# Performance work log

Hardware: AMD Instinct MI355X
Metric: run time of the kernel (lower is better)

Reference implementation:

```python
import jax, jax.numpy as jnp
import numpy as np

NUM_HEADS = 32
HEAD_DIM = 128
NUM_KV_HEADS = 8
SCALE = HEAD_DIM ** -0.5
SNAPKV_LIMIT = 512   # context.snapkv_limit
SAMPLE_Q = 128       # context.snapkv_sample_queries default
B = 4                # number of sequences (uniform length)
L = 1024             # tokens per sequence
NUM_SLOTS = 8192
NEG = jnp.float32(-1e30)


def setup_inputs() -> dict:
    key = jax.random.key(0)
    k0, k1, k2 = jax.random.split(key, 3)
    N = B * L
    q = jax.random.normal(k0, (N, NUM_HEADS, HEAD_DIM), jnp.float32)
    k = jax.random.normal(k1, (N, NUM_KV_HEADS, HEAD_DIM), jnp.float32)
    v = jax.random.normal(k2, (N, NUM_KV_HEADS, HEAD_DIM), jnp.float32)
    D = NUM_KV_HEADS * HEAD_DIM
    k_cache = jnp.zeros((NUM_SLOTS, D), jnp.float32)
    v_cache = jnp.zeros((NUM_SLOTS, D), jnp.float32)
    slot_mapping = jnp.arange(N, dtype=jnp.int32)
    cu_seqlens = jnp.arange(B + 1, dtype=jnp.int32) * L
    return dict(q=q, k=k, v=v, k_cache=k_cache, v_cache=v_cache,
                slot_mapping=slot_mapping, cu_seqlens=cu_seqlens)


def _forward(q, k, v, k_cache, v_cache, slot_mapping, cu_seqlens):
    N, H, Dh = q.shape
    Hkv = k.shape[1]
    rep = H // Hkv
    nb = cu_seqlens.shape[0] - 1
    Ls = N // nb  # uniform seq length
    qb = q.reshape(nb, Ls, H, Dh)
    kb = k.reshape(nb, Ls, Hkv, Dh)
    vb = v.reshape(nb, Ls, Hkv, Dh)

    # ---- SnapKV selection (per sequence, vectorized over batch) ----
    q_s = qb[:, Ls - SAMPLE_Q:]                       # [B, SQ, H, Dh] last queries
    k_rep = jnp.repeat(kb, rep, axis=2)               # GQA expand -> [B, L, H, Dh]
    logits = jnp.einsum('bqhd,bkhd->bhqk', q_s, k_rep) * SCALE
    abs_q = jnp.arange(Ls - SAMPLE_Q, Ls)
    abs_k = jnp.arange(Ls)
    allowed = abs_k[None, :] <= abs_q[:, None]        # [SQ, L] causal for sampled q
    logits = jnp.where(allowed[None, None], logits, NEG)
    attn = jax.nn.softmax(logits, axis=-1)
    importance = attn.sum(axis=(1, 2))                # [B, L] sum over heads+queries
    _, idx = jax.lax.top_k(importance, SNAPKV_LIMIT)
    keep_idx = jnp.sort(idx, axis=-1)                 # [B, limit] sorted kept positions

    # ---- compact KV-cache store (store_kvcache on kept tokens) ----
    kept_k = jnp.take_along_axis(kb, keep_idx[:, :, None, None], axis=1)  # [B,limit,Hkv,Dh]
    kept_v = jnp.take_along_axis(vb, keep_idx[:, :, None, None], axis=1)
    # compact slots: first num_kept (= limit) slots of each sequence
    slots = slot_mapping.reshape(nb, Ls)[:, :SNAPKV_LIMIT].reshape(-1)
    D = Hkv * Dh
    k_cache_new = k_cache.at[slots].set(kept_k.reshape(-1, D))
    v_cache_new = v_cache.at[slots].set(kept_v.reshape(-1, D))

    # ---- prefill attention (flash_attn_varlen_func, causal, raw k/v) ----
    v_rep = jnp.repeat(vb, rep, axis=2)               # [B, L, H, Dh]
    scores = jnp.einsum('bqhd,bkhd->bhqk', qb, k_rep) * SCALE
    causal = abs_k[None, :] <= abs_k[:, None]         # [L, L]
    scores = jnp.where(causal[None, None], scores, NEG)
    p = jax.nn.softmax(scores, axis=-1)
    o = jnp.einsum('bhqk,bkhd->bqhd', p, v_rep).reshape(N, H, Dh)
    return o, k_cache_new, v_cache_new


def reference(q, k, v, k_cache, v_cache, slot_mapping, cu_seqlens):
    return _forward(q, k, v, k_cache, v_cache, slot_mapping, cu_seqlens)
```

## Files before the change

kernel.cpp:

```cpp
#include <hip/hip_runtime.h>

#define B_ 4
#define L_ 1024
#define H_ 32
#define HKV_ 8
#define DH_ 128
#define SCALE_ 0.08838834764831845f
#define M_FIX 20.0f
#define KEEP_ 512
#define O_ELEMS (B_*L_*H_*DH_)
#define CACHE_ELEMS (8192*HKV_*DH_)
#define TILE_US 8192
#define QTAB_US 2097152

typedef short short8 __attribute__((ext_vector_type(8)));
typedef float floatx4 __attribute__((ext_vector_type(4)));
typedef unsigned int uintx2 __attribute__((ext_vector_type(2)));
typedef unsigned int uintx4 __attribute__((ext_vector_type(4)));

__device__ inline unsigned short bf16r(float x) {
    unsigned int u = __builtin_bit_cast(unsigned int, x);
    u += 0x7fffu + ((u >> 16) & 1u);
    return (unsigned short)(u >> 16);
}
__device__ inline unsigned int pk_bf16(float a, float b) {
    return (unsigned int)bf16r(a) | ((unsigned int)bf16r(b) << 16);
}
__device__ inline float bf16tof(unsigned short h) {
    unsigned int u = ((unsigned int)h) << 16;
    return __builtin_bit_cast(float, u);
}

__global__ __launch_bounds__(256)
void convert_kernel(const float* __restrict__ Kp, const float* __restrict__ Vp,
                    const float* __restrict__ Qp,
                    unsigned short* __restrict__ Kb, unsigned short* __restrict__ Klo,
                    unsigned short* __restrict__ VTb,
                    unsigned short* __restrict__ Qh, unsigned short* __restrict__ Ql)
{
    int bid = blockIdx.x;
    int kt = bid & 15, hkv = (bid >> 4) & 7, b = bid >> 7;
    int t = threadIdx.x;
    size_t tile = (size_t)bid * TILE_US;

    #pragma unroll
    for (int i = 0; i < 4; ++i) {
        int pos = t + 256 * i;
        int col = pos >> 4, gd = pos & 15;
        const float* kb = &Kp[((size_t)(b * L_ + kt * 64 + col) * HKV_ + hkv) * DH_ + gd * 8];
        float x[8];
        *(float4*)&x[0] = *(const float4*)kb;
        *(float4*)&x[4] = *(const float4*)(kb + 4);
        unsigned int gh[4], gl[4];
        #pragma unroll
        for (int j = 0; j < 4; ++j) {
            unsigned short h0 = bf16r(x[2*j]),   h1 = bf16r(x[2*j+1]);
            unsigned short l0 = bf16r(x[2*j]   - bf16tof(h0));
            unsigned short l1 = bf16r(x[2*j+1] - bf16tof(h1));
            gh[j] = (unsigned int)h0 | ((unsigned int)h1 << 16);
            gl[j] = (unsigned int)l0 | ((unsigned int)l1 << 16);
        }
        int phys = gd ^ (col & 15);
        *(uintx4*)&Kb[tile + col * 128 + phys * 8]  = (uintx4){gh[0], gh[1], gh[2], gh[3]};
        *(uintx4*)&Klo[tile + col * 128 + phys * 8] = (uintx4){gl[0], gl[1], gl[2], gl[3]};
    }

    {
        int d4g = t & 31, g = t >> 5;
        const float* vb = &Vp[((size_t)(b * L_ + kt * 64 + g * 8) * HKV_ + hkv) * DH_ + d4g * 4];
        const size_t vs = (size_t)HKV_ * DH_;
        float4 r[8];
        #pragma unroll
        for (int j = 0; j < 8; ++j) r[j] = *(const float4*)(vb + (size_t)j * vs);
        #pragma unroll
        for (int ii = 0; ii < 4; ++ii) {
            int d = d4g * 4 + ii;
            int phys = g ^ (d & 7);
            uintx4 gp;
            gp[0] = pk_bf16(((const float*)&r[0])[ii], ((const float*)&r[1])[ii]);
            gp[1] = pk_bf16(((const float*)&r[2])[ii], ((const float*)&r[3])[ii]);
            gp[2] = pk_bf16(((const float*)&r[4])[ii], ((const float*)&r[5])[ii]);
            gp[3] = pk_bf16(((const float*)&r[6])[ii], ((const float*)&r[7])[ii]);
            *(uintx4*)&VTb[tile + d * 64 + phys * 8] = gp;
        }
    }

    if (bid < 256) {
        int qts = bid & 1;
        int h   = (bid >> 1) & 31;
        int qb_ = bid >> 6;
        int w = t >> 6, l = t & 63, lm = l & 15, hq = l >> 4;
        int q0 = 896 + qts * 64;
        const float* qb = Qp + ((size_t)(qb_ * L_ + q0 + w * 16 + lm) * H_ + h) * DH_;
        #pragma unroll
        for (int c = 0; c < 4; ++c) {
            int dc = hq * 8 + 32 * c;
            float x[8];
            *(float4*)&x[0] = *(const float4*)(qb + dc);
            *(float4*)&x[4] = *(const float4*)(qb + dc + 4);
            short8 fh, fl;
            #pragma unroll
            for (int j = 0; j < 8; ++j) {
                float xs = x[j] * SCALE_;
                unsigned short hb = bf16r(xs);
                fh[j] = (short)hb;
                fl[j] = (short)bf16r(xs - bf16tof(hb));
            }
            size_t idx = (((size_t)bid * 4 + c) * 256 + t) * 8;
            *(short8*)&Qh[idx] = fh;
            *(short8*)&Ql[idx] = fl;
        }
    }
}

__global__ __launch_bounds__(256, 4)
void attn_mfma(const float* __restrict__ Qp, const unsigned short* __restrict__ Kbp,
               const unsigned short* __restrict__ VTp, float* __restrict__ Op)
{
    __shared__ __align__(16) unsigned short k_lds[64 * 128];
    __shared__ __align__(16) unsigned short vT[128 * 64];
    __shared__ __align__(16) unsigned short p_lds[4 * 1024];

    int bid = blockIdx.x;
    int pr = bid & 7;
    int h  = (bid >> 3) & 31;
    int b  = bid >> 8;
    int hkv = h >> 2;
    int t = threadIdx.x;
    int w = t >> 6;
    int l = t & 63;
    int lm = l & 15;
    int hq = l >> 4;

    for (int ph = 0; ph < 2; ++ph) {
        int qt = ph ? (15 - pr) : pr;

        short8 aq[4];
        {
            const float* qb = Qp + ((size_t)(b * L_ + qt * 64 + w * 16 + lm) * H_ + h) * DH_;
            #pragma unroll
            for (int c = 0; c < 4; ++c) {
                int dc = hq * 8 + 32 * c;
                float4 x0 = *(const float4*)(qb + dc);
                float4 x1 = *(const float4*)(qb + dc + 4);
                uintx4 packed;
                packed[0] = pk_bf16(x0.x * SCALE_, x0.y * SCALE_);
                packed[1] = pk_bf16(x0.z * SCALE_, x0.w * SCALE_);
                packed[2] = pk_bf16(x1.x * SCALE_, x1.y * SCALE_);
                packed[3] = pk_bf16(x1.z * SCALE_, x1.w * SCALE_);
                aq[c] = __builtin_bit_cast(short8, packed);
            }
        }

        floatx4 O[8];
        #pragma unroll
        for (int n = 0; n < 8; ++n) O[n] = (floatx4){0.f, 0.f, 0.f, 0.f};
        float l_acc[4] = {0.f, 0.f, 0.f, 0.f};

        for (int kt = 0; kt <= qt; ++kt) {
            __syncthreads();
            size_t tbase = (size_t)((b * HKV_ + hkv) * 16 + kt) * TILE_US;
            {
                const uintx4* kg = (const uintx4*)(Kbp + tbase) + t;
                const uintx4* vg = (const uintx4*)(VTp + tbase) + t;
                uintx4* kd = (uintx4*)k_lds + t;
                uintx4* vd = (uintx4*)vT + t;
                #pragma unroll
                for (int i = 0; i < 4; ++i) {
                    kd[i * 256] = kg[i * 256];
                    vd[i * 256] = vg[i * 256];
                }
            }
            __syncthreads();

            floatx4 S[4];
            #pragma unroll
            for (int c = 0; c < 4; ++c) S[c] = (floatx4){-M_FIX, -M_FIX, -M_FIX, -M_FIX};
            #pragma unroll
            for (int kc = 0; kc < 4; ++kc) {
                #pragma unroll
                for (int c = 0; c < 4; ++c) {
                    int row = lm * 4 + c;
                    int phys = (kc * 4 + hq) ^ (row & 15);
                    short8 bk = *(const short8*)&k_lds[row * 128 + phys * 8];
                    S[c] = __builtin_amdgcn_mfma_f32_16x16x32_bf16(aq[kc], bk, S[c], 0, 0, 0);
                }
            }
            bool diag = (kt == qt);
            #pragma unroll
            for (int r = 0; r < 4; ++r) {
                float e0 = __expf(S[0][r]);
                float e1 = __expf(S[1][r]);
                float e2 = __expf(S[2][r]);
                float e3 = __expf(S[3][r]);
                if (diag) {
                    int qabs = qt * 64 + w * 16 + hq * 4 + r;
                    int kb0 = kt * 64 + lm * 4;
                    e0 = (kb0 + 0 <= qabs) ? e0 : 0.f;
                    e1 = (kb0 + 1 <= qabs) ? e1 : 0.f;
                    e2 = (kb0 + 2 <= qabs) ? e2 : 0.f;
                    e3 = (kb0 + 3 <= qabs) ? e3 : 0.f;
                }
                l_acc[r] += (e0 + e1) + (e2 + e3);
                int m = hq * 4 + r;
                int phys = (lm >> 1) ^ (m & 7);
                uintx2 gp;
                gp[0] = pk_bf16(e0, e1);
                gp[1] = pk_bf16(e2, e3);
                *(uintx2*)&p_lds[w * 1024 + m * 64 + phys * 8 + (lm & 1) * 4] = gp;
            }
            asm volatile("" ::: "memory");
            int phys0 = hq ^ (lm & 7);
            int phys1 = (4 + hq) ^ (lm & 7);
            short8 bp0 = *(const short8*)&p_lds[w * 1024 + lm * 64 + phys0 * 8];
            short8 bp1 = *(const short8*)&p_lds[w * 1024 + lm * 64 + phys1 * 8];
            #pragma unroll
            for (int n = 0; n < 8; ++n) {
                int d = n * 16 + lm;
                short8 a0 = *(const short8*)&vT[d * 64 + (hq ^ (d & 7)) * 8];
                O[n] = __builtin_amdgcn_mfma_f32_16x16x32_bf16(a0, bp0, O[n], 0, 0, 0);
                short8 a1 = *(const short8*)&vT[d * 64 + (((4 + hq) ^ (d & 7))) * 8];
                O[n] = __builtin_amdgcn_mfma_f32_16x16x32_bf16(a1, bp1, O[n], 0, 0, 0);
            }
        }
        #pragma unroll
        for (int r = 0; r < 4; ++r) {
            l_acc[r] += __shfl_xor(l_acc[r], 1);
            l_acc[r] += __shfl_xor(l_acc[r], 2);
            l_acc[r] += __shfl_xor(l_acc[r], 4);
            l_acc[r] += __shfl_xor(l_acc[r], 8);
        }
        float* lf = (float*)&p_lds[w * 1024];
        if (lm == 0) {
            #pragma unroll
            for (int r = 0; r < 4; ++r) lf[hq * 4 + r] = l_acc[r];
        }
        asm volatile("" ::: "memory");
        __builtin_amdgcn_wave_barrier();
        float invl = 1.0f / lf[lm];
        #pragma unroll
        for (int n = 0; n < 8; ++n) {
            float4 res;
            res.x = O[n][0] * invl; res.y = O[n][1] * invl;
            res.z = O[n][2] * invl; res.w = O[n][3] * invl;
            *(float4*)&Op[((size_t)(b * L_ + qt * 64 + w * 16 + lm) * H_ + h) * DH_ + n * 16 + hq * 4] = res;
        }
    }
}

__global__ __launch_bounds__(256, 2)
void imp_l_kernel(const unsigned short* __restrict__ Qhp, const unsigned short* __restrict__ Qlp,
                  const unsigned short* __restrict__ Kbp, const unsigned short* __restrict__ Klop,
                  float* __restrict__ invL)
{
    __shared__ __align__(16) unsigned short khi[64 * 128];
    __shared__ __align__(16) unsigned short klo[64 * 128];

    int bid = blockIdx.x;
    int qts = bid & 1;
    int h   = (bid >> 1) & 31;
    int b   = bid >> 6;
    int hkv = h >> 2;
    int t = threadIdx.x;
    int w = t >> 6;
    int l = t & 63;
    int lm = l & 15;
    int hq = l >> 4;
    int q0 = 896 + qts * 64;
    int ktd = q0 >> 6;

    short8 aqh[4], aql[4];
    #pragma unroll
    for (int c = 0; c < 4; ++c) {
        size_t idx = (((size_t)bid * 4 + c) * 256 + t) * 8;
        aqh[c] = *(const short8*)&Qhp[idx];
        aql[c] = *(const short8*)&Qlp[idx];
    }

    float l_acc[4] = {0.f, 0.f, 0.f, 0.f};
    for (int kt = 0; kt <= ktd; ++kt) {
        __syncthreads();
        size_t tbase = (size_t)((b * HKV_ + hkv) * 16 + kt) * TILE_US;
        {
            const uintx4* hg = (const uintx4*)(Kbp + tbase) + t;
            const uintx4* lg = (const uintx4*)(Klop + tbase) + t;
            uintx4* hd = (uintx4*)khi + t;
            uintx4* ld = (uintx4*)klo + t;
            #pragma unroll
            for (int i = 0; i < 4; ++i) {
                hd[i * 256] = hg[i * 256];
                ld[i * 256] = lg[i * 256];
            }
        }
        __syncthreads();

        floatx4 S[4];
        #pragma unroll
        for (int c = 0; c < 4; ++c) S[c] = (floatx4){-M_FIX, -M_FIX, -M_FIX, -M_FIX};
        #pragma unroll
        for (int kc = 0; kc < 4; ++kc) {
            #pragma unroll
            for (int c = 0; c < 4; ++c) {
                int row = lm * 4 + c;
                int phys = (kc * 4 + hq) ^ (row & 15);
                short8 bh = *(const short8*)&khi[row * 128 + phys * 8];
                short8 bl = *(const short8*)&klo[row * 128 + phys * 8];
                S[c] = __builtin_amdgcn_mfma_f32_16x16x32_bf16(aqh[kc], bh, S[c], 0, 0, 0);
                S[c] = __builtin_amdgcn_mfma_f32_16x16x32_bf16(aqh[kc], bl, S[c], 0, 0, 0);
                S[c] = __builtin_amdgcn_mfma_f32_16x16x32_bf16(aql[kc], bh, S[c], 0, 0, 0);
            }
        }
        bool diag = (kt == ktd);
        #pragma unroll
        for (int r = 0; r < 4; ++r) {
            int qabs = q0 + w * 16 + hq * 4 + r;
            #pragma unroll
            for (int c = 0; c < 4; ++c) {
                float ev = __expf(S[c][r]);
                if (diag) {
                    int kabs = kt * 64 + lm * 4 + c;
                    ev = (kabs <= qabs) ? ev : 0.f;
                }
                l_acc[r] += ev;
            }
        }
    }
    #pragma unroll
    for (int r = 0; r < 4; ++r) {
        l_acc[r] += __shfl_xor(l_acc[r], 1);
        l_acc[r] += __shfl_xor(l_acc[r], 2);
        l_acc[r] += __shfl_xor(l_acc[r], 4);
        l_acc[r] += __shfl_xor(l_acc[r], 8);
    }
    if (lm == 0) {
        #pragma unroll
        for (int r = 0; r < 4; ++r)
            invL[((size_t)(b * H_ + h)) * 128 + qts * 64 + w * 16 + hq * 4 + r] = 1.0f / l_acc[r];
    }
}

__global__ __launch_bounds__(256, 4)
void imp_col_kernel(const unsigned short* __restrict__ Qhp, const unsigned short* __restrict__ Qlp,
                    const unsigned short* __restrict__ Kbp, const unsigned short* __restrict__ Klop,
                    const float* __restrict__ invL, float* __restrict__ imp)
{
    __shared__ __align__(16) unsigned short khi[64 * 128];
    __shared__ __align__(16) unsigned short klo[64 * 128];
    __shared__ float imp_loc[64];

    int bid = blockIdx.x;
    int kt = bid & 15;
    int h  = (bid >> 4) & 31;
    int b  = bid >> 9;
    int hkv = h >> 2;
    int t = threadIdx.x;
    int w = t >> 6;
    int l = t & 63;
    int lm = l & 15;
    int hq = l >> 4;

    if (t < 64) imp_loc[t] = 0.f;
    size_t tbase = (size_t)((b * HKV_ + hkv) * 16 + kt) * TILE_US;
    {
        const uintx4* hg = (const uintx4*)(Kbp + tbase) + t;
        const uintx4* lg = (const uintx4*)(Klop + tbase) + t;
        uintx4* hd = (uintx4*)khi + t;
        uintx4* ld = (uintx4*)klo + t;
        #pragma unroll
        for (int i = 0; i < 4; ++i) {
            hd[i * 256] = hg[i * 256];
            ld[i * 256] = lg[i * 256];
        }
    }
    __syncthreads();

    float cs[4] = {0.f, 0.f, 0.f, 0.f};
    for (int qp2 = 0; qp2 < 2; ++qp2) {
        if (kt == 15 && qp2 == 0) continue;
        int q0 = 896 + qp2 * 64;
        int qbid = (b * 32 + h) * 2 + qp2;
        short8 aqh[4], aql[4];
        #pragma unroll
        for (int c = 0; c < 4; ++c) {
            size_t idx = (((size_t)qbid * 4 + c) * 256 + t) * 8;
            aqh[c] = *(const short8*)&Qhp[idx];
            aql[c] = *(const short8*)&Qlp[idx];
        }
        floatx4 iv4 = *(const floatx4*)&invL[((size_t)(b * H_ + h)) * 128 + qp2 * 64 + w * 16 + hq * 4];

        floatx4 S[4];
        #pragma unroll
        for (int c = 0; c < 4; ++c) S[c] = (floatx4){-M_FIX, -M_FIX, -M_FIX, -M_FIX};
        #pragma unroll
        for (int kc = 0; kc < 4; ++kc) {
            #pragma unroll
            for (int c = 0; c < 4; ++c) {
                int row = lm * 4 + c;
                int phys = (kc * 4 + hq) ^ (row & 15);
                short8 bh = *(const short8*)&khi[row * 128 + phys * 8];
                short8 bl = *(const short8*)&klo[row * 128 + phys * 8];
                S[c] = __builtin_amdgcn_mfma_f32_16x16x32_bf16(aqh[kc], bh, S[c], 0, 0, 0);
                S[c] = __builtin_amdgcn_mfma_f32_16x16x32_bf16(aqh[kc], bl, S[c], 0, 0, 0);
                S[c] = __builtin_amdgcn_mfma_f32_16x16x32_bf16(aql[kc], bh, S[c], 0, 0, 0);
            }
        }
        #pragma unroll
        for (int c = 0; c < 4; ++c) {
            int kabs = kt * 64 + lm * 4 + c;
            #pragma unroll
            for (int r = 0; r < 4; ++r) {
                int qabs = q0 + w * 16 + hq * 4 + r;
                float ev = (kabs <= qabs) ? __expf(S[c][r]) : 0.f;
                cs[c] += ev * iv4[r];
            }
        }
    }
    #pragma unroll
    for (int c = 0; c < 4; ++c) {
        cs[c] += __shfl_xor(cs[c], 16);
        cs[c] += __shfl_xor(cs[c], 32);
    }
    if (l < 16) {
        #pragma unroll
        for (int c = 0; c < 4; ++c) atomicAdd(&imp_loc[lm * 4 + c], cs[c]);
    }
    __syncthreads();
    if (t < 64) atomicAdd(&imp[b * L_ + kt * 64 + t], imp_loc[t]);
}

__global__ void topk_kernel(const float* __restrict__ imp, const int* __restrict__ slot_mapping,
                            int* __restrict__ keep, int* __restrict__ inv)
{
    __shared__ float vals[1024];
    __shared__ int   idxs[1024];
    int b = blockIdx.x;
    int t = threadIdx.x;
    for (int i = t; i < 1024; i += 512) { vals[i] = imp[b * L_ + i]; idxs[i] = i; }

    for (int size = 2; size <= 1024; size <<= 1) {
        for (int stride = size >> 1; stride > 0; stride >>= 1) {
            __syncthreads();
            for (int i = t; i < 1024; i += 512) {
                int j = i ^ stride;
                if (j > i) {
                    float vi = vals[i], vj = vals[j];
                    int ii = idxs[i], ij = idxs[j];
                    bool j_before_i = (vj > vi) || (vj == vi && ij < ii);
                    bool descRegion = ((i & size) == 0);
                    bool doSwap = descRegion ? j_before_i : !j_before_i;
                    if (doSwap) {
                        vals[i] = vj; vals[j] = vi;
                        idxs[i] = ij; idxs[j] = ii;
                    }
                }
            }
        }
    }
    __syncthreads();
    for (int size = 2; size <= 512; size <<= 1) {
        for (int stride = size >> 1; stride > 0; stride >>= 1) {
            __syncthreads();
            int i = t, j = t ^ stride;
            if (j > i) {
                int a = idxs[i], bb = idxs[j];
                bool ascRegion = ((i & size) == 0);
                bool doSwap = ascRegion ? (a > bb) : (a < bb);
                if (doSwap) { idxs[i] = bb; idxs[j] = a; }
            }
        }
    }
    __syncthreads();
    keep[b * KEEP_ + t] = idxs[t];
    if (inv) {
        int dest = slot_mapping[b * L_ + t];
        inv[dest] = b * L_ + idxs[t];
    }
}

__global__ __launch_bounds__(256)
void cache_out_kernel(const float* __restrict__ kin, const float* __restrict__ vin,
                      const float* __restrict__ kc_in, const float* __restrict__ vc_in,
                      const int* __restrict__ inv,
                      float* __restrict__ kc_out, float* __restrict__ vc_out)
{
    int bid = blockIdx.x;
    int t = threadIdx.x;
    #pragma unroll
    for (int i = 0; i < 4; ++i) {
        int s = bid * 4 + i;
        int src = inv[s];
        const float4* kp = (src >= 0) ? (const float4*)&kin[(size_t)src * 1024]
                                      : (const float4*)&kc_in[(size_t)s * 1024];
        const float4* vp = (src >= 0) ? (const float4*)&vin[(size_t)src * 1024]
                                      : (const float4*)&vc_in[(size_t)s * 1024];
        ((float4*)&kc_out[(size_t)s * 1024])[t] = kp[t];
        ((float4*)&vc_out[(size_t)s * 1024])[t] = vp[t];
    }
}

__global__ __launch_bounds__(256)
void cache_copy_kernel(const float* __restrict__ kc_in, const float* __restrict__ vc_in,
                       float* __restrict__ kc_out, float* __restrict__ vc_out)
{
    size_t idx = (size_t)blockIdx.x * 256 + threadIdx.x;
    const float4* ki = (const float4*)kc_in;
    const float4* vi = (const float4*)vc_in;
    float4* ko = (float4*)kc_out;
    float4* vo = (float4*)vc_out;
    #pragma unroll
    for (int i = 0; i < 4; ++i) {
        size_t off = idx + (size_t)i * 524288;
        ko[off] = ki[off];
        vo[off] = vi[off];
    }
}

__global__ void scatter_kernel(const float* __restrict__ kin, const float* __restrict__ vin,
                               const int* __restrict__ keep, const int* __restrict__ slot_mapping,
                               float* __restrict__ kc_out, float* __restrict__ vc_out)
{
    int bid = blockIdx.x;
    int b = bid >> 9, j = bid & 511;
    int src = b * L_ + keep[b * KEEP_ + j];
    int dst = slot_mapping[b * L_ + j];
    int t = threadIdx.x;
    float4 kv = *(const float4*)&kin[(size_t)src * 1024 + t * 4];
    *(float4*)&kc_out[(size_t)dst * 1024 + t * 4] = kv;
    float4 vv = *(const float4*)&vin[(size_t)src * 1024 + t * 4];
    *(float4*)&vc_out[(size_t)dst * 1024 + t * 4] = vv;
}

extern "C" void kernel_launch(void* const* d_in, const int* in_sizes, int n_in,
                              void* d_out, int out_size, void* d_ws, size_t ws_size,
                              hipStream_t stream)
{
    const float* q = (const float*)d_in[0];
    const float* k = (const float*)d_in[1];
    const float* v = (const float*)d_in[2];
    const float* k_cache = (const float*)d_in[3];
    const float* v_cache = (const float*)d_in[4];
    const int* slot_mapping = (const int*)d_in[5];

    float* o = (float*)d_out;
    float* kc_out = o + O_ELEMS;
    float* vc_out = kc_out + CACHE_ELEMS;

    float* imp  = (float*)d_ws;
    int*   keep = (int*)(imp + B_ * L_);
    float* invL = (float*)(keep + B_ * KEEP_);
    int*   inv  = (int*)(invL + B_ * H_ * 128);
    bool use_inv = ws_size >= (size_t)(120 * 1024);
    if (!use_inv) inv = nullptr;

    const size_t SCRATCH_US = (size_t)3 * 512 * TILE_US + (size_t)2 * QTAB_US;
    bool ws_fits = ws_size >= (size_t)(128 * 1024) + SCRATCH_US * sizeof(unsigned short);
    unsigned short* Kb = ws_fits ? (unsigned short*)((char*)d_ws + 128 * 1024)
                                 : (unsigned short*)vc_out;
    unsigned short* Klo = Kb  + (size_t)512 * TILE_US;
    unsigned short* VTb = Klo + (size_t)512 * TILE_US;
    unsigned short* Qh  = VTb + (size_t)512 * TILE_US;
    unsigned short* Ql  = Qh  + (size_t)QTAB_US;

    (void)hipMemsetAsync(imp, 0, B_ * L_ * 4, stream);
    if (use_inv) (void)hipMemsetAsync(inv, 0xFF, 8192 * 4, stream);

    convert_kernel<<<dim3(512), dim3(256), 0, stream>>>(k, v, q, Kb, Klo, VTb, Qh, Ql);
    attn_mfma<<<dim3(1024), dim3(256), 0, stream>>>(q, Kb, VTb, o);
    imp_l_kernel<<<dim3(256), dim3(256), 0, stream>>>(Qh, Ql, Kb, Klo, invL);
    imp_col_kernel<<<dim3(2048), dim3(256), 0, stream>>>(Qh, Ql, Kb, Klo, invL, imp);
    topk_kernel<<<dim3(4), dim3(512), 0, stream>>>(imp, slot_mapping, keep, inv);

    if (use_inv) {
        cache_out_kernel<<<dim3(2048), dim3(256), 0, stream>>>(k, v, k_cache, v_cache, inv, kc_out, vc_out);
    } else {
        cache_copy_kernel<<<dim3(2048), dim3(256), 0, stream>>>(k_cache, v_cache, kc_out, vc_out);
        scatter_kernel<<<dim3(2048), dim3(256), 0, stream>>>(k, v, keep, slot_mapping, kc_out, vc_out);
    }
}
```

Measured before the change: 413.2 us.

## Prefetch next K/V tile in registers and split softmax row-sum over key chunks

The attention kernel now loads the next K/V tile from global memory into registers while computing on the current LDS tile, so global latency overlaps with MFMA work. Its occupancy hint moves to a waves-per-EU attribute. The SnapKV row-sum kernel is split four ways over key tiles, going from 256 to 1024 blocks, and writes partial sums that the column kernel adds and inverts. Partial sums are kept temporarily in the k-cache output region, which is overwritten later. The prefetch costs extra registers and could lower occupancy.

Result: slower. 456.3 us (+10.4%).

```diff
diff --git a/kernel.cpp b/kernel.cpp
--- a/kernel.cpp
+++ b/kernel.cpp
@@ -113,7 +113,8 @@
     }
 }
 
-__global__ __launch_bounds__(256, 4)
+__attribute__((amdgpu_waves_per_eu(4, 4)))
+__global__ __launch_bounds__(256)
 void attn_mfma(const float* __restrict__ Qp, const unsigned short* __restrict__ Kbp,
                const unsigned short* __restrict__ VTp, float* __restrict__ Op)
 {
@@ -152,6 +153,15 @@
             }
         }
 
+        uintx4 kpre[4], vpre[4];
+        {
+            size_t tb0 = (size_t)((b * HKV_ + hkv) * 16 + 0) * TILE_US;
+            const uintx4* kg = (const uintx4*)(Kbp + tb0) + t;
+            const uintx4* vg = (const uintx4*)(VTp + tb0) + t;
+            #pragma unroll
+            for (int i = 0; i < 4; ++i) { kpre[i] = kg[i * 256]; vpre[i] = vg[i * 256]; }
+        }
+
         floatx4 O[8];
         #pragma unroll
         for (int n = 0; n < 8; ++n) O[n] = (floatx4){0.f, 0.f, 0.f, 0.f};
@@ -159,19 +169,20 @@
 
         for (int kt = 0; kt <= qt; ++kt) {
             __syncthreads();
-            size_t tbase = (size_t)((b * HKV_ + hkv) * 16 + kt) * TILE_US;
             {
-                const uintx4* kg = (const uintx4*)(Kbp + tbase) + t;
-                const uintx4* vg = (const uintx4*)(VTp + tbase) + t;
                 uintx4* kd = (uintx4*)k_lds + t;
                 uintx4* vd = (uintx4*)vT + t;
                 #pragma unroll
-                for (int i = 0; i < 4; ++i) {
-                    kd[i * 256] = kg[i * 256];
-                    vd[i * 256] = vg[i * 256];
-                }
+                for (int i = 0; i < 4; ++i) { kd[i * 256] = kpre[i]; vd[i * 256] = vpre[i]; }
             }
             __syncthreads();
+            if (kt < qt) {
+                size_t tb = (size_t)((b * HKV_ + hkv) * 16 + kt + 1) * TILE_US;
+                const uintx4* kg = (const uintx4*)(Kbp + tb) + t;
+                const uintx4* vg = (const uintx4*)(VTp + tb) + t;
+                #pragma unroll
+                for (int i = 0; i < 4; ++i) { kpre[i] = kg[i * 256]; vpre[i] = vg[i * 256]; }
+            }
 
             floatx4 S[4];
             #pragma unroll
@@ -248,19 +259,21 @@
     }
 }
 
-__global__ __launch_bounds__(256, 2)
-void imp_l_kernel(const unsigned short* __restrict__ Qhp, const unsigned short* __restrict__ Qlp,
-                  const unsigned short* __restrict__ Kbp, const unsigned short* __restrict__ Klop,
-                  float* __restrict__ invL)
+__global__ __launch_bounds__(256)
+void imp_lsum_kernel(const unsigned short* __restrict__ Qhp, const unsigned short* __restrict__ Qlp,
+                     const unsigned short* __restrict__ Kbp, const unsigned short* __restrict__ Klop,
+                     float* __restrict__ lpart)
 {
     __shared__ __align__(16) unsigned short khi[64 * 128];
     __shared__ __align__(16) unsigned short klo[64 * 128];
 
     int bid = blockIdx.x;
-    int qts = bid & 1;
-    int h   = (bid >> 1) & 31;
-    int b   = bid >> 6;
+    int chunk = bid & 3;
+    int qts = (bid >> 2) & 1;
+    int h   = (bid >> 3) & 31;
+    int b   = bid >> 8;
     int hkv = h >> 2;
+    int qblock = (b * 32 + h) * 2 + qts;
     int t = threadIdx.x;
     int w = t >> 6;
     int l = t & 63;
@@ -268,17 +281,19 @@
     int hq = l >> 4;
     int q0 = 896 + qts * 64;
     int ktd = q0 >> 6;
+    int kt_lo = chunk * 4;
+    int kt_hi = min(kt_lo + 3, ktd);
 
     short8 aqh[4], aql[4];
     #pragma unroll
     for (int c = 0; c < 4; ++c) {
-        size_t idx = (((size_t)bid * 4 + c) * 256 + t) * 8;
+        size_t idx = (((size_t)qblock * 4 + c) * 256 + t) * 8;
         aqh[c] = *(const short8*)&Qhp[idx];
         aql[c] = *(const short8*)&Qlp[idx];
     }
 
     float l_acc[4] = {0.f, 0.f, 0.f, 0.f};
-    for (int kt = 0; kt <= ktd; ++kt) {
+    for (int kt = kt_lo; kt <= kt_hi; ++kt) {
         __syncthreads();
         size_t tbase = (size_t)((b * HKV_ + hkv) * 16 + kt) * TILE_US;
         {
@@ -334,15 +349,17 @@
     }
     if (lm == 0) {
         #pragma unroll
-        for (int r = 0; r < 4; ++r)
-            invL[((size_t)(b * H_ + h)) * 128 + qts * 64 + w * 16 + hq * 4 + r] = 1.0f / l_acc[r];
+        for (int r = 0; r < 4; ++r) {
+            int row = w * 16 + hq * 4 + r;
+            lpart[((size_t)qblock * 64 + row) * 4 + chunk] = l_acc[r];
+        }
     }
 }
 
 __global__ __launch_bounds__(256, 4)
 void imp_col_kernel(const unsigned short* __restrict__ Qhp, const unsigned short* __restrict__ Qlp,
                     const unsigned short* __restrict__ Kbp, const unsigned short* __restrict__ Klop,
-                    const float* __restrict__ invL, float* __restrict__ imp)
+                    const float* __restrict__ lpart, float* __restrict__ imp)
 {
     __shared__ __align__(16) unsigned short khi[64 * 128];
     __shared__ __align__(16) unsigned short klo[64 * 128];
@@ -377,8 +394,8 @@
     float cs[4] = {0.f, 0.f, 0.f, 0.f};
     for (int qp2 = 0; qp2 < 2; ++qp2) {
         if (kt == 15 && qp2 == 0) continue;
+        int qbid = (b * 32 + h) * 2 + qp2;
         int q0 = 896 + qp2 * 64;
-        int qbid = (b * 32 + h) * 2 + qp2;
         short8 aqh[4], aql[4];
         #pragma unroll
         for (int c = 0; c < 4; ++c) {
@@ -386,7 +403,13 @@
             aqh[c] = *(const short8*)&Qhp[idx];
             aql[c] = *(const short8*)&Qlp[idx];
         }
-        floatx4 iv4 = *(const floatx4*)&invL[((size_t)(b * H_ + h)) * 128 + qp2 * 64 + w * 16 + hq * 4];
+        floatx4 iv4;
+        #pragma unroll
+        for (int r = 0; r < 4; ++r) {
+            int row = w * 16 + hq * 4 + r;
+            float4 p = *(const float4*)&lpart[((size_t)qbid * 64 + row) * 4];
+            iv4[r] = 1.0f / ((p.x + p.y) + (p.z + p.w));
+        }
 
         floatx4 S[4];
         #pragma unroll
@@ -552,6 +575,8 @@
     bool use_inv = ws_size >= (size_t)(120 * 1024);
     if (!use_inv) inv = nullptr;
 
+    float* lpart = kc_out;
+
     const size_t SCRATCH_US = (size_t)3 * 512 * TILE_US + (size_t)2 * QTAB_US;
     bool ws_fits = ws_size >= (size_t)(128 * 1024) + SCRATCH_US * sizeof(unsigned short);
     unsigned short* Kb = ws_fits ? (unsigned short*)((char*)d_ws + 128 * 1024)
@@ -566,8 +591,8 @@
 
     convert_kernel<<<dim3(512), dim3(256), 0, stream>>>(k, v, q, Kb, Klo, VTb, Qh, Ql);
     attn_mfma<<<dim3(1024), dim3(256), 0, stream>>>(q, Kb, VTb, o);
-    imp_l_kernel<<<dim3(256), dim3(256), 0, stream>>>(Qh, Ql, Kb, Klo, invL);
-    imp_col_kernel<<<dim3(2048), dim3(256), 0, stream>>>(Qh, Ql, Kb, Klo, invL, imp);
+    imp_lsum_kernel<<<dim3(1024), dim3(256), 0, stream>>>(Qh, Ql, Kb, Klo, lpart);
+    imp_col_kernel<<<dim3(2048), dim3(256), 0, stream>>>(Qh, Ql, Kb, Klo, lpart, imp);
     topk_kernel<<<dim3(4), dim3(512), 0, stream>>>(imp, slot_mapping, keep, inv);
 
     if (use_inv) {
```
